# Kernel tuning notes

Hardware: AMD Instinct MI355X
Metric: run time of the kernel (lower is better)

The kernel has to match this reference:

```python
import jax, jax.numpy as jnp
import numpy as np

N_HEAD, N_KV, HEAD_DIM, GATE_CH = 16, 4, 128, 32

def _rope(x, cos, sin):
    d = x.shape[3] // 2
    x1, x2 = x[..., :d], x[..., d:]
    return jnp.concatenate([x1 * cos + x2 * sin, x1 * (-sin) + x2 * cos], axis=3)

def _rmsnorm(x):
    xf = x.astype(jnp.float32)
    return (x * jax.lax.rsqrt(jnp.mean(xf * xf, axis=-1, keepdims=True) + 1e-6)).astype(x.dtype)

def setup_inputs() -> dict:
    key = jax.random.key(0)
    ks = jax.random.split(key, 9)
    B, T, C = 2, 2048, 2048
    return {
        "x":  jax.random.normal(ks[0], (B, T, C), jnp.float32),
        "ve": jax.random.normal(ks[1], (B, T, N_KV * HEAD_DIM), jnp.float32),
        "cos": jax.random.uniform(ks[2], (T, 1, HEAD_DIM // 2), jnp.float32),
        "sin": jax.random.uniform(ks[3], (T, 1, HEAD_DIM // 2), jnp.float32),
        "Wq": jax.random.normal(ks[4], (C, N_HEAD * HEAD_DIM), jnp.float32) * 0.02,
        "Wk": jax.random.normal(ks[5], (C, N_KV * HEAD_DIM), jnp.float32) * 0.02,
        "Wv": jax.random.normal(ks[6], (C, N_KV * HEAD_DIM), jnp.float32) * 0.02,
        "Wg": jax.random.normal(ks[7], (GATE_CH, N_KV), jnp.float32) * 0.02,
        "Wo": jax.random.normal(ks[8], (C, C), jnp.float32) * 0.02,
        "window": 1024,
    }

def reference(x, ve, cos, sin, Wq, Wk, Wv, Wg, Wo, window):
    B, T, C = x.shape
    q = (x @ Wq).reshape(B, T, N_HEAD, HEAD_DIM)
    k = (x @ Wk).reshape(B, T, N_KV, HEAD_DIM)
    v = (x @ Wv).reshape(B, T, N_KV, HEAD_DIM)
    # value-embedding gate (ve_gate active for this layer)
    gate = 2.0 * jax.nn.sigmoid(x[..., :GATE_CH] @ Wg)  # (B,T,N_KV)
    v = v + gate[..., None] * ve.reshape(B, T, N_KV, HEAD_DIM)
    q, k = _rope(q, cos, sin), _rope(k, cos, sin)
    q, k = _rmsnorm(q), _rmsnorm(k)
    # GQA: repeat kv heads (repeat_interleave over head dim)
    groups = N_HEAD // N_KV
    k = jnp.repeat(k, groups, axis=2)
    v = jnp.repeat(v, groups, axis=2)
    scale = 1.0 / np.sqrt(HEAD_DIM)
    scores = jnp.einsum("bthd,bshd->bhts", q, k) * scale  # (B,H,T,T)
    idx = jnp.arange(T)
    diff = idx[None, :] - idx[:, None]  # diff[i,j] = j - i, as in torch code
    mask = (diff >= 0) & (diff < window)
    scores = jnp.where(mask[None, None], scores, -jnp.inf)
    p = jax.nn.softmax(scores, axis=-1)
    y = jnp.einsum("bhts,bshd->bthd", p, v).reshape(B, T, C)
    return y @ Wo
```

## Files before the change

### kernel.cpp

```cpp
#include <hip/hip_runtime.h>
#include <hip/hip_bf16.h>
#include <cstdint>

typedef __hip_bfloat16 bf16;
typedef __attribute__((ext_vector_type(8))) short short8;
typedef __attribute__((ext_vector_type(4))) short short4v;
typedef __attribute__((ext_vector_type(4))) float f32x4;

#define T_   2048
#define CDIM 2048
#define NH   16
#define NKV  4
#define HD   128
#define QSCALE (0.08838834764831845f * 1.44269504088896340f)

__device__ __forceinline__ void gload_lds16(const void* g, void* l) {
  __builtin_amdgcn_global_load_lds(
      (const __attribute__((address_space(1))) void*)g,
      (__attribute__((address_space(3))) void*)l, 16, 0, 0);
}

template <int G> __device__ __forceinline__ void vm_gate() {
  if constexpr (G == 5)      asm volatile("s_waitcnt vmcnt(5)" ::: "memory");
  else if constexpr (G == 4) asm volatile("s_waitcnt vmcnt(4)" ::: "memory");
  else if constexpr (G == 3) asm volatile("s_waitcnt vmcnt(3)" ::: "memory");
  else                       asm volatile("s_waitcnt vmcnt(0)" ::: "memory");
}

__global__ __launch_bounds__(256) void prep_kernel(
    const float* __restrict__ x, const float* __restrict__ Wq,
    const float* __restrict__ Wk, const float* __restrict__ Wv,
    const float* __restrict__ Wo, ushort4* __restrict__ xb,
    bf16* __restrict__ wT, bf16* __restrict__ woT) {
  int b = blockIdx.x;
  if (b < 8192) {
    int i = b * 256 + threadIdx.x;
    float4 v = ((const float4*)x)[i];
    union { bf16 h[4]; ushort4 u; } cv;
    cv.h[0] = __float2bfloat16(v.x);
    cv.h[1] = __float2bfloat16(v.y);
    cv.h[2] = __float2bfloat16(v.z);
    cv.h[3] = __float2bfloat16(v.w);
    xb[i] = cv.u;
    return;
  }
  const float* W; bf16* WT; int N, nbx, idx;
  if (b < 12288)      { W = Wq; WT = wT;                       N = 2048; nbx = 64; idx = b - 8192; }
  else if (b < 13312) { W = Wk; WT = wT + (size_t)2048 * 2048; N = 512;  nbx = 16; idx = b - 12288; }
  else if (b < 14336) { W = Wv; WT = wT + (size_t)2560 * 2048; N = 512;  nbx = 16; idx = b - 13312; }
  else                { W = Wo; WT = woT;                      N = 2048; nbx = 64; idx = b - 14336; }
  __shared__ float tile[32][33];
  const int K = 2048;
  int n0 = (idx % nbx) * 32, k0 = (idx / nbx) * 32;
  int r = threadIdx.x >> 5, c = threadIdx.x & 31;
  for (int i = 0; i < 4; ++i)
    tile[r + i * 8][c] = W[(size_t)(k0 + r + i * 8) * N + n0 + c];
  __syncthreads();
  for (int i = 0; i < 4; ++i)
    WT[(size_t)(n0 + r + i * 8) * K + k0 + c] = __float2bfloat16(tile[c][r + i * 8]);
}

template <int MH, int NF, typename CT>
__global__ __launch_bounds__(512, 2) void gemm_q4(const bf16* __restrict__ A,
                                                  const bf16* __restrict__ BT,
                                                  CT* __restrict__ C,
                                                  int N, int K, int RY, int RX) {
  constexpr int BM = MH * 32;
  constexpr int BN = NF * 64;
  constexpr int MQ = MH / 2;
  constexpr int ALOADS = (MH + 3) / 4;
  constexpr int NB0 = (NF + 1) / 2;
  constexpr int NB1 = NF - NB0;
  constexpr int GATE = NF + ALOADS;
  __shared__ __align__(16) bf16 sA[2][BM * 64];
  __shared__ __align__(16) bf16 sB[2][BN * 64];

  int tid = threadIdx.x;
  int lane = tid & 63, w = tid >> 6;
  int wm = w >> 2, wn = w & 3;
  int lr = lane & 15, lk = lane >> 4;

  int xcd = blockIdx.x & 7, t = blockIdx.x >> 3;
  int by = (xcd >> 1) * RY + t / RX;
  int bx = (xcd & 1) * RX + t % RX;
  int m0 = by * BM, n0 = bx * BN;

  f32x4 acc[MH][NF];
#pragma unroll
  for (int m = 0; m < MH; ++m)
#pragma unroll
    for (int n = 0; n < NF; ++n) acc[m][n] = (f32x4){0.f, 0.f, 0.f, 0.f};

  const bf16* Abase = A + (size_t)m0 * K;
  const bf16* Bbase = BT + (size_t)n0 * K;

  auto stB = [&](int p, int kt) {
    int kb = kt << 6;
#pragma unroll
    for (int i = 0; i < NF; ++i) {
      int c = i * 512 + tid;
      int r = c >> 3, sl = c & 7;
      gload_lds16(Bbase + (size_t)r * K + kb + ((sl ^ (r & 7)) << 3),
                  (char*)(&sB[p][0]) + c * 16);
    }
  };
  auto stA = [&](int p, int kt, int h) {
    int kb = kt << 6;
#pragma unroll
    for (int i = 0; i < ALOADS; ++i) {
      int c = i * 512 + tid;
      int r = (c >> 3) + h * (BM / 2), sl = c & 7;
      gload_lds16(Abase + (size_t)r * K + kb + ((sl ^ (r & 7)) << 3),
                  (char*)(&sA[p][0]) + r * 128 + sl * 16);
    }
  };

  int nk = K >> 6;
  stB(0, 0); stA(0, 0, 0); stA(0, 0, 1);
  stB(1, 1); stA(1, 1, 0);
  vm_gate<GATE>();
  __builtin_amdgcn_s_barrier();

#define READ_AF(DST, QM)                                                   \
  {                                                                        \
    _Pragma("unroll")                                                      \
    for (int mi = 0; mi < MQ; ++mi) {                                      \
      int row = wm * (MH * 16) + (QM) * (MQ * 16) + mi * 16 + lr;          \
      const char* rb = sAb + row * 128;                                    \
      int rx = (row & 7) << 4;                                             \
      DST[mi][0] = *(const short8*)(rb + ((lk * 16) ^ rx));                \
      DST[mi][1] = *(const short8*)(rb + ((64 + lk * 16) ^ rx));           \
    }                                                                      \
  }
#define READ_BF(DST, FBASE, CNT)                                           \
  {                                                                        \
    _Pragma("unroll")                                                      \
    for (int f = 0; f < (CNT); ++f) {                                      \
      int row = wn * (NF * 16) + ((FBASE) + f) * 16 + lr;                  \
      const char* rb = sBb + row * 128;                                    \
      int rx = (row & 7) << 4;                                             \
      DST[f][0] = *(const short8*)(rb + ((lk * 16) ^ rx));                 \
      DST[f][1] = *(const short8*)(rb + ((64 + lk * 16) ^ rx));            \
    }                                                                      \
  }
#define MFMA_Q(AF, BF, QM, FBASE, CNT)                                     \
  __builtin_amdgcn_s_setprio(1);                                           \
  _Pragma("unroll")                                                        \
  for (int kk = 0; kk < 2; ++kk)                                           \
    _Pragma("unroll")                                                      \
    for (int mi = 0; mi < MQ; ++mi)                                        \
      _Pragma("unroll")                                                    \
      for (int f = 0; f < (CNT); ++f)                                      \
        acc[(QM) * MQ + mi][(FBASE) + f] =                                 \
            __builtin_amdgcn_mfma_f32_16x16x32_bf16(                       \
                AF[mi][kk], BF[f][kk], acc[(QM) * MQ + mi][(FBASE) + f],   \
                0, 0, 0);                                                  \
  __builtin_amdgcn_s_setprio(0);
#define RD_SYNC                                                            \
  __builtin_amdgcn_s_barrier();                                            \
  asm volatile("s_waitcnt lgkmcnt(0)" ::: "memory");                       \
  __builtin_amdgcn_sched_barrier(0);

  for (int kt = 0; kt < nk; ++kt) {
    int p = kt & 1;
    const char* sAb = (const char*)(&sA[p][0]);
    const char* sBb = (const char*)(&sB[p][0]);
    short8 af0[MQ][2], af1[MQ][2], bf0[NB0][2], bf1[NB1][2];

    READ_AF(af0, 0);
    READ_BF(bf0, 0, NB0);
    if (kt + 1 < nk) stA(p ^ 1, kt + 1, 1);
    RD_SYNC;
    MFMA_Q(af0, bf0, 0, 0, NB0);
    __builtin_amdgcn_s_barrier();

    READ_BF(bf1, NB0, NB1);
    RD_SYNC;
    MFMA_Q(af0, bf1, 0, NB0, NB1);
    __builtin_amdgcn_s_barrier();

    READ_AF(af1, 1);
    if (kt + 2 < nk) stB(p, kt + 2);
    RD_SYNC;
    MFMA_Q(af1, bf1, 1, NB0, NB1);
    __builtin_amdgcn_s_barrier();

    if (kt + 2 < nk) stA(p, kt + 2, 0);
    MFMA_Q(af1, bf0, 1, 0, NB0);
    if (kt + 2 < nk) vm_gate<GATE>();
    else             vm_gate<0>();
    __builtin_amdgcn_s_barrier();
  }
#undef READ_AF
#undef READ_BF
#undef MFMA_Q
#undef RD_SYNC

#pragma unroll
  for (int m = 0; m < MH; ++m)
#pragma unroll
    for (int n = 0; n < NF; ++n)
#pragma unroll
      for (int jj = 0; jj < 4; ++jj) {
        size_t idx = (size_t)(m0 + wm * (MH * 16) + (m / MQ) * (MQ * 16) +
                              (m % MQ) * 16 + lk * 4 + jj) * N +
                     n0 + wn * (NF * 16) + n * 16 + lr;
        if constexpr (__is_same(CT, float))
          C[idx] = acc[m][n][jj];
        else
          C[idx] = __float2bfloat16(acc[m][n][jj]);
      }
}

__global__ __launch_bounds__(256) void epilogue_kernel(
    const bf16* __restrict__ qkv, const float* __restrict__ x,
    const float* __restrict__ ve, const float* __restrict__ cosT,
    const float* __restrict__ sinT, const float* __restrict__ Wg,
    bf16* __restrict__ qn, bf16* __restrict__ kn, bf16* __restrict__ vT) {
  int row = blockIdx.x;
  int bi = row >> 11, t = row & 2047;
  int tid = threadIdx.x, lane = tid & 63, w = tid >> 6;
  __shared__ float gate[NKV];
  size_t rb = (size_t)row * 3072;

  if (tid < 128) {
    int g = tid >> 5, i = tid & 31;
    float p = x[(size_t)row * CDIM + i] * Wg[i * 4 + g];
    p += __shfl_xor(p, 1);  p += __shfl_xor(p, 2);
    p += __shfl_xor(p, 4);  p += __shfl_xor(p, 8);
    p += __shfl_xor(p, 16);
    if (i == 0) gate[g] = 2.f / (1.f + __expf(-p));
  }
  __syncthreads();

  float cv = cosT[t * 64 + lane];
  float sv = sinT[t * 64 + lane];

  for (int it = 0; it < 4; ++it) {
    int h = it * 4 + w;
    float x1 = __bfloat162float(qkv[rb + h * 128 + lane]);
    float x2 = __bfloat162float(qkv[rb + h * 128 + 64 + lane]);
    float y1 = x1 * cv + x2 * sv;
    float y2 = x2 * cv - x1 * sv;
    float ss = y1 * y1 + y2 * y2;
    ss += __shfl_xor(ss, 1);  ss += __shfl_xor(ss, 2);  ss += __shfl_xor(ss, 4);
    ss += __shfl_xor(ss, 8);  ss += __shfl_xor(ss, 16); ss += __shfl_xor(ss, 32);
    float r = rsqrtf(ss * (1.f / 128.f) + 1e-6f) * QSCALE;
    size_t ob = (size_t)row * (NH * HD) + h * 128;
    qn[ob + lane] = __float2bfloat16(y1 * r);
    qn[ob + 64 + lane] = __float2bfloat16(y2 * r);
  }
  {
    int h = w;
    float x1 = __bfloat162float(qkv[rb + 2048 + h * 128 + lane]);
    float x2 = __bfloat162float(qkv[rb + 2048 + h * 128 + 64 + lane]);
    float y1 = x1 * cv + x2 * sv;
    float y2 = x2 * cv - x1 * sv;
    float ss = y1 * y1 + y2 * y2;
    ss += __shfl_xor(ss, 1);  ss += __shfl_xor(ss, 2);  ss += __shfl_xor(ss, 4);
    ss += __shfl_xor(ss, 8);  ss += __shfl_xor(ss, 16); ss += __shfl_xor(ss, 32);
    float r = rsqrtf(ss * (1.f / 128.f) + 1e-6f);
    size_t ob = (size_t)row * (NKV * HD) + h * 128;
    kn[ob + lane] = __float2bfloat16(y1 * r);
    kn[ob + 64 + lane] = __float2bfloat16(y2 * r);
  }
  for (int e = tid; e < 512; e += 256) {
    int kv = e >> 7, d = e & 127;
    float val = __bfloat162float(qkv[rb + 2560 + e]) + gate[kv] * ve[(size_t)row * 512 + e];
    vT[((size_t)(bi * NKV + kv) * HD + d) * T_ + t] = __float2bfloat16(val);
  }
}

__global__ __launch_bounds__(256, 2) void attn_kernel(
    const bf16* __restrict__ qn, const bf16* __restrict__ kn,
    const bf16* __restrict__ vT, bf16* __restrict__ y,
    const int* __restrict__ winp) {
  __shared__ __align__(16) bf16 sK[2][64 * 128];
  __shared__ __align__(16) bf16 sV[2][128 * 64];

  int win = *winp;
  int id = blockIdx.x;
  int g  = id & 7;
  int bi = g >> 2, kvh = g & 3;
  int rem = id >> 3;
  int h  = kvh * 4 + (rem & 3);
  int q0 = (rem >> 2) << 7;
  int tid = threadIdx.x;
  int lane = tid & 63, w = tid >> 6;
  int lr = lane & 15, lk = lane >> 4;

  short8 qfA[4], qfB[4];
  {
    const bf16* qrA = qn + (size_t)(bi * T_ + q0 + w * 32 + lr) * (NH * HD) + h * HD;
    const bf16* qrB = qrA + (size_t)16 * (NH * HD);
#pragma unroll
    for (int c = 0; c < 4; ++c) {
      qfA[c] = *(const short8*)(qrA + c * 32 + lk * 8);
      qfB[c] = *(const short8*)(qrB + c * 32 + lk * 8);
    }
  }

  int kge[4], klb[4], vge[4], vlbA[4], vlbB[4];
#pragma unroll
  for (int i = 0; i < 4; ++i) {
    int c = i * 256 + tid;
    int kr = c >> 4, ks = c & 15;
    kge[i] = kr * (NKV * HD) + ks * 8;
    klb[i] = kr * 256 + ((ks ^ (kr & 7)) << 4);
    int vr = c >> 3, vs = c & 7;
    vge[i] = vr * T_ + vs * 8;
    int hh = vs >> 2, m = vs & 3, a = m >> 1;
    int sA = 8 * ((2 * m) & 3) + 4 * a;
    int sB = 8 * ((2 * m + 1) & 3) + 4 * a;
    int tA = 64 * hh + 2 * sA, tB = 64 * hh + 2 * sB;
    vlbA[i] = vr * 128 + (((tA >> 4) ^ (vr & 7)) << 4) + (tA & 15);
    vlbB[i] = vr * 128 + (((tB >> 4) ^ (vr & 7)) << 4) + (tB & 15);
  }
  const bf16* kpane = kn + (size_t)bi * T_ * (NKV * HD) + kvh * HD;
  const bf16* vpane = vT + (size_t)(bi * NKV + kvh) * HD * T_;

  short8 kreg[4], vreg[4];
  auto LOAD = [&](int jtx) {
    const bf16* kb = kpane + (size_t)(jtx << 6) * (NKV * HD);
    const bf16* vb = vpane + (jtx << 6);
#pragma unroll
    for (int i = 0; i < 4; ++i) kreg[i] = *(const short8*)(kb + kge[i]);
#pragma unroll
    for (int i = 0; i < 4; ++i) vreg[i] = *(const short8*)(vb + vge[i]);
  };
  auto WRITE = [&](int b) {
    char* kBuf = (char*)(&sK[b][0]);
    char* vBuf = (char*)(&sV[b][0]);
#pragma unroll
    for (int i = 0; i < 4; ++i) *(short8*)(kBuf + klb[i]) = kreg[i];
#pragma unroll
    for (int i = 0; i < 4; ++i) {
      union { short8 s8; short4v s4[2]; } u;
      u.s8 = vreg[i];
      *(short4v*)(vBuf + vlbA[i]) = u.s4[0];
      *(short4v*)(vBuf + vlbB[i]) = u.s4[1];
    }
  };

  f32x4 o0[8], o1[8];
#pragma unroll
  for (int i = 0; i < 8; ++i) {
    o0[i] = (f32x4){0.f, 0.f, 0.f, 0.f};
    o1[i] = (f32x4){0.f, 0.f, 0.f, 0.f};
  }
  float lp0 = 0.f, lp1 = 0.f;

  int jt0 = q0 >> 6;
  int hi = q0 + 126 + win; if (hi > T_ - 1) hi = T_ - 1;
  int jt1 = hi >> 6;

  LOAD(jt0);
  WRITE(0);
  if (jt0 < jt1) LOAD(jt0 + 1);
  asm volatile("s_waitcnt lgkmcnt(0)\n\ts_barrier" ::: "memory");

  int irow0 = q0 + w * 32 + lr;
  int klo = lk * 4;

  int p = 0;
  for (int jt = jt0; jt <= jt1; ++jt) {
    int j0 = jt << 6;

    if (jt < jt1) {
      WRITE(p ^ 1);
      if (jt + 1 < jt1) LOAD(jt + 2);
    }

    const char* sKb = (const char*)(&sK[p][0]);
    const char* sVb = (const char*)(&sV[p][0]);

    f32x4 s0[4], s1[4];
#pragma unroll
    for (int sub = 0; sub < 4; ++sub) {
      s0[sub] = (f32x4){0.f, 0.f, 0.f, 0.f};
      s1[sub] = (f32x4){0.f, 0.f, 0.f, 0.f};
    }
    __builtin_amdgcn_s_setprio(1);
#pragma unroll
    for (int sub = 0; sub < 4; ++sub) {
      int kr = sub * 16 + lr;
      int rx = (kr & 7) << 4;
      const char* rowb = sKb + kr * 256;
#pragma unroll
      for (int c = 0; c < 4; ++c) {
        short8 kf = *(const short8*)(rowb + ((c * 64 + lk * 16) ^ rx));
        s0[sub] = __builtin_amdgcn_mfma_f32_16x16x32_bf16(kf, qfA[c], s0[sub], 0, 0, 0);
        s1[sub] = __builtin_amdgcn_mfma_f32_16x16x32_bf16(kf, qfB[c], s1[sub], 0, 0, 0);
      }
    }
    __builtin_amdgcn_s_setprio(0);

    bool full = (j0 >= q0 + 128) && (j0 + 64 <= q0 + win);
    int koff0 = j0 - irow0;
    int koff1 = koff0 - 16;

    short8 pA0, pA1, pB0, pB1;
    {
      unsigned pk[8];
#pragma unroll
      for (int sub = 0; sub < 4; ++sub) {
        float p0 = exp2f(s0[sub][0]), p1 = exp2f(s0[sub][1]);
        float p2 = exp2f(s0[sub][2]), p3 = exp2f(s0[sub][3]);
        if (!full) {
          int base = koff0 + sub * 16 + klo;
          p0 = ((unsigned)(base + 0) < (unsigned)win) ? p0 : 0.f;
          p1 = ((unsigned)(base + 1) < (unsigned)win) ? p1 : 0.f;
          p2 = ((unsigned)(base + 2) < (unsigned)win) ? p2 : 0.f;
          p3 = ((unsigned)(base + 3) < (unsigned)win) ? p3 : 0.f;
        }
        lp0 += (p0 + p1) + (p2 + p3);
        asm("v_cvt_pk_bf16_f32 %0, %1, %2" : "=v"(pk[sub * 2])     : "v"(p0), "v"(p1));
        asm("v_cvt_pk_bf16_f32 %0, %1, %2" : "=v"(pk[sub * 2 + 1]) : "v"(p2), "v"(p3));
      }
      union { unsigned u[4]; short8 s8; } c0, c1;
      c0.u[0] = pk[0]; c0.u[1] = pk[1]; c0.u[2] = pk[2]; c0.u[3] = pk[3];
      c1.u[0] = pk[4]; c1.u[1] = pk[5]; c1.u[2] = pk[6]; c1.u[3] = pk[7];
      pA0 = c0.s8; pA1 = c1.s8;
    }
    {
      unsigned pk[8];
#pragma unroll
      for (int sub = 0; sub < 4; ++sub) {
        float p0 = exp2f(s1[sub][0]), p1 = exp2f(s1[sub][1]);
        float p2 = exp2f(s1[sub][2]), p3 = exp2f(s1[sub][3]);
        if (!full) {
          int base = koff1 + sub * 16 + klo;
          p0 = ((unsigned)(base + 0) < (unsigned)win) ? p0 : 0.f;
          p1 = ((unsigned)(base + 1) < (unsigned)win) ? p1 : 0.f;
          p2 = ((unsigned)(base + 2) < (unsigned)win) ? p2 : 0.f;
          p3 = ((unsigned)(base + 3) < (unsigned)win) ? p3 : 0.f;
        }
        lp1 += (p0 + p1) + (p2 + p3);
        asm("v_cvt_pk_bf16_f32 %0, %1, %2" : "=v"(pk[sub * 2])     : "v"(p0), "v"(p1));
        asm("v_cvt_pk_bf16_f32 %0, %1, %2" : "=v"(pk[sub * 2 + 1]) : "v"(p2), "v"(p3));
      }
      union { unsigned u[4]; short8 s8; } c0, c1;
      c0.u[0] = pk[0]; c0.u[1] = pk[1]; c0.u[2] = pk[2]; c0.u[3] = pk[3];
      c1.u[0] = pk[4]; c1.u[1] = pk[5]; c1.u[2] = pk[6]; c1.u[3] = pk[7];
      pB0 = c0.s8; pB1 = c1.s8;
    }

    __builtin_amdgcn_s_setprio(1);
#pragma unroll
    for (int nb = 0; nb < 8; ++nb) {
      int vr = nb * 16 + lr;
      int vrx = (vr & 7) << 4;
      const char* vb = sVb + vr * 128;
      short8 vf0 = *(const short8*)(vb + ((lk * 16) ^ vrx));
      short8 vf1 = *(const short8*)(vb + ((64 + lk * 16) ^ vrx));
      o0[nb] = __builtin_amdgcn_mfma_f32_16x16x32_bf16(pA0, vf0, o0[nb], 0, 0, 0);
      o0[nb] = __builtin_amdgcn_mfma_f32_16x16x32_bf16(pA1, vf1, o0[nb], 0, 0, 0);
      o1[nb] = __builtin_amdgcn_mfma_f32_16x16x32_bf16(pB0, vf0, o1[nb], 0, 0, 0);
      o1[nb] = __builtin_amdgcn_mfma_f32_16x16x32_bf16(pB1, vf1, o1[nb], 0, 0, 0);
    }
    __builtin_amdgcn_s_setprio(0);

    asm volatile("s_waitcnt lgkmcnt(0)\n\ts_barrier" ::: "memory");
    p ^= 1;
  }

  float l0 = lp0, l1 = lp1;
  l0 += __shfl_xor(l0, 16); l0 += __shfl_xor(l0, 32);
  l1 += __shfl_xor(l1, 16); l1 += __shfl_xor(l1, 32);
#pragma unroll
  for (int jj = 0; jj < 4; ++jj) {
    float inv0 = 1.f / __shfl(l0, klo + jj);
    float inv1 = 1.f / __shfl(l1, klo + jj);
    size_t ob0 = (size_t)(bi * T_ + q0 + w * 32 + klo + jj) * (NH * HD) + h * HD;
    size_t ob1 = ob0 + (size_t)16 * (NH * HD);
#pragma unroll
    for (int nb = 0; nb < 8; ++nb) {
      y[ob0 + nb * 16 + lr] = __float2bfloat16(o0[nb][jj] * inv0);
      y[ob1 + nb * 16 + lr] = __float2bfloat16(o1[nb][jj] * inv1);
    }
  }
}

extern "C" void kernel_launch(void* const* d_in, const int* in_sizes, int n_in,
                              void* d_out, int out_size, void* d_ws, size_t ws_size,
                              hipStream_t stream) {
  const float* x    = (const float*)d_in[0];
  const float* ve   = (const float*)d_in[1];
  const float* cosT = (const float*)d_in[2];
  const float* sinT = (const float*)d_in[3];
  const float* Wq   = (const float*)d_in[4];
  const float* Wk   = (const float*)d_in[5];
  const float* Wv   = (const float*)d_in[6];
  const float* Wg   = (const float*)d_in[7];
  const float* Wo   = (const float*)d_in[8];
  const int*   win  = (const int*)d_in[9];
  float* out = (float*)d_out;

  char* ws = (char*)d_ws;
  bf16*  xb   = (bf16*)(ws);
  bf16*  wT   = (bf16*)(ws + 16777216);
  bf16*  woT  = (bf16*)(ws + 29360128);
  bf16*  qkvb = (bf16*)(ws + 37748736);
  bf16*  qn   = (bf16*)(ws + 62914560);
  bf16*  kn   = (bf16*)(ws + 79691776);
  bf16*  vTb  = (bf16*)(ws + 83886080);
  bf16*  y    = qkvb;

  prep_kernel<<<18432, 256, 0, stream>>>(x, Wq, Wk, Wv, Wo, (ushort4*)xb, wT, woT);

  gemm_q4<4, 3, bf16><<<512, 512, 0, stream>>>(xb, wT, qkvb, 3072, 2048, 8, 8);
  epilogue_kernel<<<4096, 256, 0, stream>>>(qkvb, x, ve, cosT, sinT, Wg, qn, kn, vTb);
  attn_kernel<<<512, 256, 0, stream>>>(qn, kn, vTb, y, win);
  gemm_q4<4, 2, float><<<512, 512, 0, stream>>>(y, woT, out, 2048, 2048, 8, 8);
}
```

Measured before the change: 175.1 us.

## Fuse RoPE, RMSNorm and value-gate epilogue into QKV GEMM

Replaces the separate QKV GEMM and per-row epilogue kernel with one GEMM using 128x128 tiles. Each tile is staged through LDS and gets RoPE/RMSNorm (Q,K) or the gated value-embedding add and transpose (V) applied in place. The gate sigmoid is moved into extra blocks of the prep kernel. This drops the bf16 QKV intermediate round trip and one launch, at the cost of a different tile shape (768 blocks of 128x128 instead of 512 of 128x192) and an LDS epilogue with strided vT stores.

```diff
diff --git a/kernel.cpp b/kernel.cpp
--- a/kernel.cpp
+++ b/kernel.cpp
@@ -30,8 +30,9 @@
 __global__ __launch_bounds__(256) void prep_kernel(
     const float* __restrict__ x, const float* __restrict__ Wq,
     const float* __restrict__ Wk, const float* __restrict__ Wv,
-    const float* __restrict__ Wo, ushort4* __restrict__ xb,
-    bf16* __restrict__ wT, bf16* __restrict__ woT) {
+    const float* __restrict__ Wo, const float* __restrict__ Wg,
+    ushort4* __restrict__ xb, bf16* __restrict__ wT, bf16* __restrict__ woT,
+    float* __restrict__ gate4) {
   int b = blockIdx.x;
   if (b < 8192) {
     int i = b * 256 + threadIdx.x;
@@ -42,6 +43,18 @@
     cv.h[2] = __float2bfloat16(v.z);
     cv.h[3] = __float2bfloat16(v.w);
     xb[i] = cv.u;
+    return;
+  }
+  if (b >= 18432) {
+    int idx = b - 18432;
+    int row = idx * 2 + (threadIdx.x >> 7);
+    int tt = threadIdx.x & 127;
+    int g = tt >> 5, i = tt & 31;
+    float p = x[(size_t)row * CDIM + i] * Wg[i * 4 + g];
+    p += __shfl_xor(p, 1);  p += __shfl_xor(p, 2);
+    p += __shfl_xor(p, 4);  p += __shfl_xor(p, 8);
+    p += __shfl_xor(p, 16);
+    if (i == 0) gate4[row * 4 + g] = 2.f / (1.f + __expf(-p));
     return;
   }
   const float* W; bf16* WT; int N, nbx, idx;
@@ -58,6 +71,195 @@
   __syncthreads();
   for (int i = 0; i < 4; ++i)
     WT[(size_t)(n0 + r + i * 8) * K + k0 + c] = __float2bfloat16(tile[c][r + i * 8]);
+}
+
+__global__ __launch_bounds__(512, 2) void gemm_qkvf(
+    const bf16* __restrict__ A, const bf16* __restrict__ BT,
+    const float* __restrict__ ve, const float* __restrict__ cosT,
+    const float* __restrict__ sinT, const float* __restrict__ gate4,
+    bf16* __restrict__ qn, bf16* __restrict__ kn, bf16* __restrict__ vT) {
+  __shared__ __align__(16) char smem[65536];
+  const int K = 2048;
+
+  int tid = threadIdx.x;
+  int lane = tid & 63, w = tid >> 6;
+  int wm = w >> 2, wn = w & 3;
+  int lr = lane & 15, lk = lane >> 4;
+
+  int xcd = blockIdx.x & 7, t = blockIdx.x >> 3;
+  int by = (xcd >> 1) * 8 + t / 12;
+  int bx = (xcd & 1) * 12 + t % 12;
+  int m0 = by * 128, n0 = bx * 128;
+
+  f32x4 acc[4][2];
+#pragma unroll
+  for (int m = 0; m < 4; ++m)
+#pragma unroll
+    for (int n = 0; n < 2; ++n) acc[m][n] = (f32x4){0.f, 0.f, 0.f, 0.f};
+
+  const bf16* Abase = A + (size_t)m0 * K;
+  const bf16* Bbase = BT + (size_t)n0 * K;
+
+  auto sAp = [&](int p) { return smem + p * 16384; };
+  auto sBp = [&](int p) { return smem + 32768 + p * 16384; };
+
+  auto stB = [&](int p, int kt) {
+    int kb = kt << 6;
+#pragma unroll
+    for (int i = 0; i < 2; ++i) {
+      int c = i * 512 + tid;
+      int r = c >> 3, sl = c & 7;
+      gload_lds16(Bbase + (size_t)r * K + kb + ((sl ^ (r & 7)) << 3),
+                  sBp(p) + c * 16);
+    }
+  };
+  auto stA = [&](int p, int kt, int h) {
+    int kb = kt << 6;
+    int c = tid;
+    int r = (c >> 3) + h * 64, sl = c & 7;
+    gload_lds16(Abase + (size_t)r * K + kb + ((sl ^ (r & 7)) << 3),
+                sAp(p) + r * 128 + sl * 16);
+  };
+
+  int nk = K >> 6;
+  stB(0, 0); stA(0, 0, 0); stA(0, 0, 1);
+  stB(1, 1); stA(1, 1, 0);
+  vm_gate<3>();
+  __builtin_amdgcn_s_barrier();
+
+#define READ_AF(DST, QM)                                                   \
+  {                                                                        \
+    _Pragma("unroll")                                                      \
+    for (int mi = 0; mi < 2; ++mi) {                                       \
+      int row = wm * 64 + (QM) * 32 + mi * 16 + lr;                        \
+      const char* rb = sAb + row * 128;                                    \
+      int rx = (row & 7) << 4;                                             \
+      DST[mi][0] = *(const short8*)(rb + ((lk * 16) ^ rx));                \
+      DST[mi][1] = *(const short8*)(rb + ((64 + lk * 16) ^ rx));           \
+    }                                                                      \
+  }
+#define READ_BF(DST, FB)                                                   \
+  {                                                                        \
+    int row = wn * 32 + (FB) * 16 + lr;                                    \
+    const char* rb = sBb + row * 128;                                      \
+    int rx = (row & 7) << 4;                                               \
+    DST[0][0] = *(const short8*)(rb + ((lk * 16) ^ rx));                   \
+    DST[0][1] = *(const short8*)(rb + ((64 + lk * 16) ^ rx));              \
+  }
+#define MFMA_Q(AF, BF, QM, FB)                                             \
+  __builtin_amdgcn_s_setprio(1);                                           \
+  _Pragma("unroll")                                                        \
+  for (int kk = 0; kk < 2; ++kk)                                           \
+    _Pragma("unroll")                                                      \
+    for (int mi = 0; mi < 2; ++mi)                                         \
+      acc[(QM) * 2 + mi][FB] = __builtin_amdgcn_mfma_f32_16x16x32_bf16(    \
+          AF[mi][kk], BF[0][kk], acc[(QM) * 2 + mi][FB], 0, 0, 0);         \
+  __builtin_amdgcn_s_setprio(0);
+#define RD_SYNC                                                            \
+  __builtin_amdgcn_s_barrier();                                            \
+  asm volatile("s_waitcnt lgkmcnt(0)" ::: "memory");                       \
+  __builtin_amdgcn_sched_barrier(0);
+
+  for (int kt = 0; kt < nk; ++kt) {
+    int p = kt & 1;
+    const char* sAb = (const char*)sAp(p);
+    const char* sBb = (const char*)sBp(p);
+    short8 af0[2][2], af1[2][2], bf0[1][2], bf1[1][2];
+
+    READ_AF(af0, 0);
+    READ_BF(bf0, 0);
+    if (kt + 1 < nk) stA(p ^ 1, kt + 1, 1);
+    RD_SYNC;
+    MFMA_Q(af0, bf0, 0, 0);
+    __builtin_amdgcn_s_barrier();
+
+    READ_BF(bf1, 1);
+    RD_SYNC;
+    MFMA_Q(af0, bf1, 0, 1);
+    __builtin_amdgcn_s_barrier();
+
+    READ_AF(af1, 1);
+    if (kt + 2 < nk) stB(p, kt + 2);
+    RD_SYNC;
+    MFMA_Q(af1, bf1, 1, 1);
+    __builtin_amdgcn_s_barrier();
+
+    if (kt + 2 < nk) stA(p, kt + 2, 0);
+    MFMA_Q(af1, bf0, 1, 0);
+    if (kt + 2 < nk) vm_gate<3>();
+    else             vm_gate<0>();
+    __builtin_amdgcn_s_barrier();
+  }
+#undef READ_AF
+#undef READ_BF
+#undef MFMA_Q
+#undef RD_SYNC
+
+  float* tl = (float*)smem;
+#pragma unroll
+  for (int m = 0; m < 4; ++m)
+#pragma unroll
+    for (int n = 0; n < 2; ++n)
+#pragma unroll
+      for (int jj = 0; jj < 4; ++jj) {
+        int row = wm * 64 + (m >> 1) * 32 + (m & 1) * 16 + lk * 4 + jj;
+        int col = wn * 32 + n * 16 + lr;
+        tl[row * 128 + col] = acc[m][n][jj];
+      }
+  __syncthreads();
+
+  if (bx < 16) {
+    size_t hb = (size_t)bx * 128;
+    for (int it = 0; it < 16; ++it) {
+      int row = it * 8 + w;
+      int grow = m0 + row;
+      int tk = grow & (T_ - 1);
+      float x1 = tl[row * 128 + lane];
+      float x2 = tl[row * 128 + 64 + lane];
+      float cv = cosT[tk * 64 + lane], sv = sinT[tk * 64 + lane];
+      float y1 = x1 * cv + x2 * sv;
+      float y2 = x2 * cv - x1 * sv;
+      float ss = y1 * y1 + y2 * y2;
+      ss += __shfl_xor(ss, 1);  ss += __shfl_xor(ss, 2);  ss += __shfl_xor(ss, 4);
+      ss += __shfl_xor(ss, 8);  ss += __shfl_xor(ss, 16); ss += __shfl_xor(ss, 32);
+      float r = rsqrtf(ss * (1.f / 128.f) + 1e-6f) * QSCALE;
+      qn[(size_t)grow * (NH * HD) + hb + lane]      = __float2bfloat16(y1 * r);
+      qn[(size_t)grow * (NH * HD) + hb + 64 + lane] = __float2bfloat16(y2 * r);
+    }
+  } else if (bx < 20) {
+    size_t hb = (size_t)(bx - 16) * 128;
+    for (int it = 0; it < 16; ++it) {
+      int row = it * 8 + w;
+      int grow = m0 + row;
+      int tk = grow & (T_ - 1);
+      float x1 = tl[row * 128 + lane];
+      float x2 = tl[row * 128 + 64 + lane];
+      float cv = cosT[tk * 64 + lane], sv = sinT[tk * 64 + lane];
+      float y1 = x1 * cv + x2 * sv;
+      float y2 = x2 * cv - x1 * sv;
+      float ss = y1 * y1 + y2 * y2;
+      ss += __shfl_xor(ss, 1);  ss += __shfl_xor(ss, 2);  ss += __shfl_xor(ss, 4);
+      ss += __shfl_xor(ss, 8);  ss += __shfl_xor(ss, 16); ss += __shfl_xor(ss, 32);
+      float r = rsqrtf(ss * (1.f / 128.f) + 1e-6f);
+      kn[(size_t)grow * (NKV * HD) + hb + lane]      = __float2bfloat16(y1 * r);
+      kn[(size_t)grow * (NKV * HD) + hb + 64 + lane] = __float2bfloat16(y2 * r);
+    }
+  } else {
+    int kv = bx - 20;
+    for (int it = 0; it < 16; ++it) {
+      int row = it * 8 + w;
+      int grow = m0 + row;
+      int tk = grow & (T_ - 1);
+      int bi = grow >> 11;
+      float g = gate4[grow * 4 + kv];
+      const float* vep = ve + (size_t)grow * (NKV * HD) + kv * 128;
+      float v1 = tl[row * 128 + lane]      + g * vep[lane];
+      float v2 = tl[row * 128 + 64 + lane] + g * vep[64 + lane];
+      size_t vb = (size_t)(bi * NKV + kv) * 128;
+      vT[(vb + lane) * T_ + tk]      = __float2bfloat16(v1);
+      vT[(vb + 64 + lane) * T_ + tk] = __float2bfloat16(v2);
+    }
+  }
 }
 
 template <int MH, int NF, typename CT>
@@ -210,65 +412,6 @@
         else
           C[idx] = __float2bfloat16(acc[m][n][jj]);
       }
-}
-
-__global__ __launch_bounds__(256) void epilogue_kernel(
-    const bf16* __restrict__ qkv, const float* __restrict__ x,
-    const float* __restrict__ ve, const float* __restrict__ cosT,
-    const float* __restrict__ sinT, const float* __restrict__ Wg,
-    bf16* __restrict__ qn, bf16* __restrict__ kn, bf16* __restrict__ vT) {
-  int row = blockIdx.x;
-  int bi = row >> 11, t = row & 2047;
-  int tid = threadIdx.x, lane = tid & 63, w = tid >> 6;
-  __shared__ float gate[NKV];
-  size_t rb = (size_t)row * 3072;
-
-  if (tid < 128) {
-    int g = tid >> 5, i = tid & 31;
-    float p = x[(size_t)row * CDIM + i] * Wg[i * 4 + g];
-    p += __shfl_xor(p, 1);  p += __shfl_xor(p, 2);
-    p += __shfl_xor(p, 4);  p += __shfl_xor(p, 8);
-    p += __shfl_xor(p, 16);
-    if (i == 0) gate[g] = 2.f / (1.f + __expf(-p));
-  }
-  __syncthreads();
-
-  float cv = cosT[t * 64 + lane];
-  float sv = sinT[t * 64 + lane];
-
-  for (int it = 0; it < 4; ++it) {
-    int h = it * 4 + w;
-    float x1 = __bfloat162float(qkv[rb + h * 128 + lane]);
-    float x2 = __bfloat162float(qkv[rb + h * 128 + 64 + lane]);
-    float y1 = x1 * cv + x2 * sv;
-    float y2 = x2 * cv - x1 * sv;
-    float ss = y1 * y1 + y2 * y2;
-    ss += __shfl_xor(ss, 1);  ss += __shfl_xor(ss, 2);  ss += __shfl_xor(ss, 4);
-    ss += __shfl_xor(ss, 8);  ss += __shfl_xor(ss, 16); ss += __shfl_xor(ss, 32);
-    float r = rsqrtf(ss * (1.f / 128.f) + 1e-6f) * QSCALE;
-    size_t ob = (size_t)row * (NH * HD) + h * 128;
-    qn[ob + lane] = __float2bfloat16(y1 * r);
-    qn[ob + 64 + lane] = __float2bfloat16(y2 * r);
-  }
-  {
-    int h = w;
-    float x1 = __bfloat162float(qkv[rb + 2048 + h * 128 + lane]);
-    float x2 = __bfloat162float(qkv[rb + 2048 + h * 128 + 64 + lane]);
-    float y1 = x1 * cv + x2 * sv;
-    float y2 = x2 * cv - x1 * sv;
-    float ss = y1 * y1 + y2 * y2;
-    ss += __shfl_xor(ss, 1);  ss += __shfl_xor(ss, 2);  ss += __shfl_xor(ss, 4);
-    ss += __shfl_xor(ss, 8);  ss += __shfl_xor(ss, 16); ss += __shfl_xor(ss, 32);
-    float r = rsqrtf(ss * (1.f / 128.f) + 1e-6f);
-    size_t ob = (size_t)row * (NKV * HD) + h * 128;
-    kn[ob + lane] = __float2bfloat16(y1 * r);
-    kn[ob + 64 + lane] = __float2bfloat16(y2 * r);
-  }
-  for (int e = tid; e < 512; e += 256) {
-    int kv = e >> 7, d = e & 127;
-    float val = __bfloat162float(qkv[rb + 2560 + e]) + gate[kv] * ve[(size_t)row * 512 + e];
-    vT[((size_t)(bi * NKV + kv) * HD + d) * T_ + t] = __float2bfloat16(val);
-  }
 }
 
 __global__ __launch_bounds__(256, 2) void attn_kernel(
@@ -497,19 +640,18 @@
   float* out = (float*)d_out;
 
   char* ws = (char*)d_ws;
-  bf16*  xb   = (bf16*)(ws);
-  bf16*  wT   = (bf16*)(ws + 16777216);
-  bf16*  woT  = (bf16*)(ws + 29360128);
-  bf16*  qkvb = (bf16*)(ws + 37748736);
-  bf16*  qn   = (bf16*)(ws + 62914560);
-  bf16*  kn   = (bf16*)(ws + 79691776);
-  bf16*  vTb  = (bf16*)(ws + 83886080);
-  bf16*  y    = qkvb;
-
-  prep_kernel<<<18432, 256, 0, stream>>>(x, Wq, Wk, Wv, Wo, (ushort4*)xb, wT, woT);
-
-  gemm_q4<4, 3, bf16><<<512, 512, 0, stream>>>(xb, wT, qkvb, 3072, 2048, 8, 8);
-  epilogue_kernel<<<4096, 256, 0, stream>>>(qkvb, x, ve, cosT, sinT, Wg, qn, kn, vTb);
+  bf16*  xb    = (bf16*)(ws);
+  bf16*  wT    = (bf16*)(ws + 16777216);
+  bf16*  woT   = (bf16*)(ws + 29360128);
+  bf16*  qn    = (bf16*)(ws + 37748736);
+  bf16*  kn    = (bf16*)(ws + 54525952);
+  bf16*  vTb   = (bf16*)(ws + 58720256);
+  bf16*  y     = (bf16*)(ws + 62914560);
+  float* gate4 = (float*)(ws + 79691776);
+
+  prep_kernel<<<20480, 256, 0, stream>>>(x, Wq, Wk, Wv, Wo, Wg,
+                                         (ushort4*)xb, wT, woT, gate4);
+  gemm_qkvf<<<768, 512, 0, stream>>>(xb, wT, ve, cosT, sinT, gate4, qn, kn, vTb);
   attn_kernel<<<512, 256, 0, stream>>>(qn, kn, vTb, y, win);
   gemm_q4<4, 2, float><<<512, 512, 0, stream>>>(y, woT, out, 2048, 2048, 8, 8);
 }
```

After: 202.5 us. +15.7%, slower.
